# Kernel optimization log

Hardware: AMD Instinct MI355X
Metric: run time of the kernel (lower is better)

## Reference

```python
import jax, jax.numpy as jnp
import numpy as np
import math

B, S, D_MODEL = 4, 2048, 1024
H, D_QK, D_V = 16, 64, 64


def setup_inputs() -> dict:
    key = jax.random.key(0)
    ks = jax.random.split(key, 12)
    s = 0.02
    return {
        "input_q": jax.random.normal(ks[0], (B, S, D_MODEL), jnp.float32),
        "input_k": jax.random.normal(ks[1], (B, S, D_MODEL), jnp.float32),
        "input_v": jax.random.normal(ks[2], (B, S, D_MODEL), jnp.float32),
        # per-head projection weights stacked over heads: [H, out, d_model] (torch Linear layout)
        "WQw": jax.random.normal(ks[3], (H, D_QK, D_MODEL), jnp.float32) * s,
        "WQb": jax.random.normal(ks[4], (H, D_QK), jnp.float32) * s,
        "WKw": jax.random.normal(ks[5], (H, D_QK, D_MODEL), jnp.float32) * s,
        "WKb": jax.random.normal(ks[6], (H, D_QK), jnp.float32) * s,
        "WVw": jax.random.normal(ks[7], (H, D_V, D_MODEL), jnp.float32) * s,
        "WVb": jax.random.normal(ks[8], (H, D_V), jnp.float32) * s,
        # output projection: Linear(H*D_V, D_MODEL)
        "Ww": jax.random.normal(ks[9], (D_MODEL, H * D_V), jnp.float32) * s,
        "Wb": jax.random.normal(ks[10], (D_MODEL,), jnp.float32) * s,
    }


def _mha(input_q, input_k, input_v, WQw, WQb, WKw, WKb, WVw, WVb, Ww, Wb):
    # per-head projections: [B,H,S,d]
    Q = jnp.einsum("bsd,hed->bhse", input_q, WQw) + WQb[None, :, None, :]
    K = jnp.einsum("bsd,hed->bhse", input_k, WKw) + WKb[None, :, None, :]
    V = jnp.einsum("bsd,hvd->bhsv", input_v, WVw) + WVb[None, :, None, :]
    scores = jnp.einsum("bhse,bhte->bhst", Q, K)  # [B,H,S,S]
    # causal mask added BEFORE division by sqrt(d_model), as in original
    causal = jnp.triu(jnp.full((S, S), -jnp.inf, scores.dtype), k=1)
    scores = (scores + causal) / math.sqrt(D_MODEL)  # NOTE: d_model, not d_qk
    attn = jax.nn.softmax(scores, axis=-1)
    ctx = jnp.einsum("bhst,bhtv->bhsv", attn, V)  # [B,H,S,D_V]
    concat = ctx.transpose(0, 2, 1, 3).reshape(B, S, H * D_V)  # head-order concat
    return concat @ Ww.T + Wb


def reference(input_q, input_k, input_v, WQw, WQb, WKw, WKb, WVw, WVb, Ww, Wb):
    return _mha(input_q, input_k, input_v, WQw, WQb, WKw, WKb, WVw, WVb, Ww, Wb)
```

## Files before the change

### kernel.cpp

```cpp
#include <hip/hip_runtime.h>
#include <hip/hip_bf16.h>

typedef __attribute__((ext_vector_type(8))) short bf16x8;
typedef __attribute__((ext_vector_type(4))) float f32x4;
typedef __attribute__((ext_vector_type(16))) float f32x16;
typedef __attribute__((ext_vector_type(4))) unsigned uint4v;

#define MFMA16(a, b, c) __builtin_amdgcn_mfma_f32_16x16x32_bf16(a, b, c, 0, 0, 0)
#define MFMA32(a, b, c) __builtin_amdgcn_mfma_f32_32x32x16_bf16(a, b, c, 0, 0, 0)

__device__ __forceinline__ unsigned short f2bfn(float f) {
#if defined(__gfx950__)
  __bf16 h = (__bf16)f;
  return __builtin_bit_cast(unsigned short, h);
#else
  union { float f; unsigned u; } x; x.f = f;
  unsigned r = x.u + 0x7fffu + ((x.u >> 16) & 1u);
  return (unsigned short)(r >> 16);
#endif
}

__device__ __forceinline__ unsigned cvtpk(float lo, float hi) {
  unsigned w;
  asm("v_cvt_pk_bf16_f32 %0, %1, %2" : "=v"(w) : "v"(lo), "v"(hi));
  return w;
}

__device__ __forceinline__ void cvt_range(const float* __restrict__ s,
                                          unsigned short* __restrict__ d,
                                          int i, int st, int n8) {
  for (; i < n8; i += st) {
    const float4* sp = reinterpret_cast<const float4*>(s) + 2 * (size_t)i;
    float4 a = sp[0], b = sp[1];
    uint4v o;
    o[0] = cvtpk(a.x, a.y); o[1] = cvtpk(a.z, a.w);
    o[2] = cvtpk(b.x, b.y); o[3] = cvtpk(b.z, b.w);
    reinterpret_cast<uint4v*>(d)[i] = o;
  }
}

__global__ void cvt1_kernel(const float* __restrict__ s, unsigned short* __restrict__ d, int n8) {
  cvt_range(s, d, blockIdx.x * blockDim.x + threadIdx.x, gridDim.x * blockDim.x, n8);
}

__global__ void cvt_first_kernel(const float* s0, const float* s1, const float* s2,
                                 const float* s3, unsigned short* d0, unsigned short* d1,
                                 unsigned short* d2, unsigned short* d3, int wn8,
                                 const float* sq, unsigned short* dq, int qn8) {
  const float* s; unsigned short* d; int n8;
  switch (blockIdx.y) {
    case 0: s = s0; d = d0; n8 = wn8; break;
    case 1: s = s1; d = d1; n8 = wn8; break;
    case 2: s = s2; d = d2; n8 = wn8; break;
    case 3: s = s3; d = d3; n8 = wn8; break;
    default: s = sq; d = dq; n8 = qn8; break;
  }
  cvt_range(s, d, blockIdx.x * blockDim.x + threadIdx.x, gridDim.x * blockDim.x, n8);
}

template <int MODE>
__global__ __launch_bounds__(256) void gemm_kernel(
    const unsigned short* __restrict__ Av, const unsigned short* __restrict__ Bv,
    const float* __restrict__ bias, void* __restrict__ outv,
    int M, int N, int K, float oscale, int nshift, int ngemm,
    const float* __restrict__ csrc, unsigned short* __restrict__ cdst, int cn8) {
  constexpr int BM = 128, BN = 128, BK = 64;
  __shared__ __align__(16) unsigned short As[2][BM * BK];
  __shared__ __align__(16) unsigned short Bs[2][BN * BK];
  const int bx = blockIdx.x;
  const int tid = threadIdx.x;
  if (bx >= ngemm) {
    cvt_range(csrc, cdst, (bx - ngemm) * blockDim.x + tid,
              (gridDim.x - ngemm) * blockDim.x, cn8);
    return;
  }
  int sx = bx;
  if (nshift == 3) sx = (bx & 7) * (ngemm >> 3) + (bx >> 3);
  const int lane = tid & 63, wave = tid >> 6;
  const int wr = wave >> 1, wc = wave & 1;
  const int m0 = (sx >> nshift) * BM, n0 = (sx & ((1 << nshift) - 1)) * BN;
  const int rb = lane & 15, g = lane >> 4;
  const int swz = ((lane & 7) ^ ((lane >> 3) & 7)) * 8;
  f32x4 acc[4][4] = {};

  const unsigned short* Ab = Av + (size_t)m0 * K;
  const unsigned short* Bb = Bv + (size_t)n0 * K;

  auto stage = [&](int buf, int k0) {
#pragma unroll
    for (int i = 0; i < 4; ++i) {
      const int c = wave * 256 + i * 64 + lane;
      const int r = c >> 3;
      __builtin_amdgcn_global_load_lds(
          (const __attribute__((address_space(1))) unsigned int*)(Ab + (size_t)r * K + k0 + swz),
          (__attribute__((address_space(3))) unsigned int*)&As[buf][c * 8], 16, 0, 0);
      __builtin_amdgcn_global_load_lds(
          (const __attribute__((address_space(1))) unsigned int*)(Bb + (size_t)r * K + k0 + swz),
          (__attribute__((address_space(3))) unsigned int*)&Bs[buf][c * 8], 16, 0, 0);
    }
  };

  const int nt = K / BK;
  stage(0, 0);
  int cur = 0;
  for (int t = 0; t < nt; ++t) {
    __syncthreads();
    if (t + 1 < nt) stage(cur ^ 1, (t + 1) * BK);
    const unsigned short* A_ = As[cur];
    const unsigned short* B_ = Bs[cur];
#pragma unroll
    for (int kc = 0; kc < 2; ++kc) {
      bf16x8 af[4], bfr[4];
#pragma unroll
      for (int mi = 0; mi < 4; ++mi)
        af[mi] = *reinterpret_cast<const bf16x8*>(
            &A_[(wr * 64 + mi * 16 + rb) * 64 + (((kc * 4 + g) ^ (rb & 7)) * 8)]);
#pragma unroll
      for (int ni = 0; ni < 4; ++ni)
        bfr[ni] = *reinterpret_cast<const bf16x8*>(
            &B_[(wc * 64 + ni * 16 + rb) * 64 + (((kc * 4 + g) ^ (rb & 7)) * 8)]);
#pragma unroll
      for (int mi = 0; mi < 4; ++mi)
#pragma unroll
        for (int ni = 0; ni < 4; ++ni)
          acc[mi][ni] = MFMA16(af[mi], bfr[ni], acc[mi][ni]);
    }
    cur ^= 1;
  }

#pragma unroll
  for (int mi = 0; mi < 4; ++mi) {
#pragma unroll
    for (int ni = 0; ni < 4; ++ni) {
      int col = n0 + wc * 64 + ni * 16 + rb;
      if constexpr (MODE != 2) {
        float bvv = bias[col];
#pragma unroll
        for (int j = 0; j < 4; ++j) {
          int row = m0 + wr * 64 + mi * 16 + g * 4 + j;
          float v = acc[mi][ni][j] + bvv;
          if constexpr (MODE == 0) {
            v *= oscale;
            int b = row >> 11, s = row & 2047;
            int h = col >> 6, e = col & 63;
            ((unsigned short*)outv)[((size_t)(b * 16 + h) * 2048 + s) * 64 + e] = f2bfn(v);
          } else {
            ((float*)outv)[(size_t)row * N + col] = v;
          }
        }
      } else {
        int bb = col >> 11, s = col & 2047;
#pragma unroll
        for (int j = 0; j < 4; ++j) {
          int row = m0 + wr * 64 + mi * 16 + g * 4 + j;
          float v = acc[mi][ni][j] + bias[row];
          int h = row >> 6, e = row & 63;
          ((unsigned short*)outv)[((size_t)(bb * 16 + h) * 64 + e) * 2048 + s] = f2bfn(v);
        }
      }
    }
  }
}

__global__ __launch_bounds__(256) void attn7_kernel(
    const unsigned short* __restrict__ Qp, const unsigned short* __restrict__ Kp,
    const unsigned short* __restrict__ Vtp, unsigned short* __restrict__ ctx) {
  constexpr int S = 2048;
  __shared__ __align__(16) unsigned short Ks[2][64 * 64];
  __shared__ __align__(16) unsigned short Vs[2][64 * 64];
  const int bx = blockIdx.x;
  const int bh = bx & 63;
  const int qti = 15 - (bx >> 6);
  const int tid = threadIdx.x, wave = tid >> 6, lane = tid & 63;
  const int l31 = lane & 31, hb = lane >> 5;
  const int x7 = l31 & 7;
  const int qw = qti * 128 + wave * 32;
  const unsigned short* Qb = Qp + (size_t)bh * S * 64;
  const unsigned short* Kb = Kp + (size_t)bh * S * 64;
  const unsigned short* Vb = Vtp + (size_t)bh * 64 * S;

  bf16x8 qg[4];
#pragma unroll
  for (int kc = 0; kc < 4; ++kc)
    qg[kc] = *reinterpret_cast<const bf16x8*>(
        Qb + (size_t)(qw + l31) * 64 + 16 * kc + 8 * hb);

  bf16x8 ones;
#pragma unroll
  for (int i = 0; i < 8; ++i) ones[i] = (short)0x3F80;

  f32x16 ls = {};
  f32x16 o[2] = {};
  const int sswz = ((lane & 7) ^ (lane >> 3)) * 8;
  const int nt = qti * 2 + 2;

  const int ci0 = wave * 2 * 64 + lane, ci1 = ci0 + 64;
  const int r0 = wave * 16 + (lane >> 3), r1 = r0 + 8;
  const int rs0 = (r0 & 51) | ((r0 & 4) << 1) | ((r0 & 8) >> 1);
  const int rs1 = (r1 & 51) | ((r1 & 4) << 1) | ((r1 & 8) >> 1);
  const unsigned short* ks0 = Kb + (size_t)rs0 * 64 + sswz;
  const unsigned short* ks1 = Kb + (size_t)rs1 * 64 + sswz;
  const unsigned short* vs0 = Vb + (size_t)r0 * S + sswz;
  const unsigned short* vs1 = Vb + (size_t)r1 * S + sswz;

  auto stage = [&](int buf) {
    __builtin_amdgcn_global_load_lds(
        (const __attribute__((address_space(1))) unsigned int*)ks0,
        (__attribute__((address_space(3))) unsigned int*)&Ks[buf][ci0 * 8], 16, 0, 0);
    __builtin_amdgcn_global_load_lds(
        (const __attribute__((address_space(1))) unsigned int*)ks1,
        (__attribute__((address_space(3))) unsigned int*)&Ks[buf][ci1 * 8], 16, 0, 0);
    __builtin_amdgcn_global_load_lds(
        (const __attribute__((address_space(1))) unsigned int*)vs0,
        (__attribute__((address_space(3))) unsigned int*)&Vs[buf][ci0 * 8], 16, 0, 0);
    __builtin_amdgcn_global_load_lds(
        (const __attribute__((address_space(1))) unsigned int*)vs1,
        (__attribute__((address_space(3))) unsigned int*)&Vs[buf][ci1 * 8], 16, 0, 0);
    ks0 += 4096; ks1 += 4096;
    vs0 += 64; vs1 += 64;
  };

  stage(0);

  for (int it = 0; it < nt; ++it) {
    __syncthreads();
    if (it + 1 < nt) stage((it + 1) & 1);
    const int kv0 = 64 * it;
    if (kv0 <= qw + 31) {
      const unsigned short* K_ = Ks[it & 1];
      const unsigned short* V_ = Vs[it & 1];
      f32x16 sacc[2] = {};
      __builtin_amdgcn_s_setprio(1);
#pragma unroll
      for (int kc = 0; kc < 4; ++kc) {
        bf16x8 kf0 = *reinterpret_cast<const bf16x8*>(
            &K_[l31 * 64 + ((2 * kc + hb) ^ x7) * 8]);
        bf16x8 kf1 = *reinterpret_cast<const bf16x8*>(
            &K_[(32 + l31) * 64 + ((2 * kc + hb) ^ x7) * 8]);
        sacc[0] = MFMA32(kf0, qg[kc], sacc[0]);
        sacc[1] = MFMA32(kf1, qg[kc], sacc[1]);
      }
      __builtin_amdgcn_s_setprio(0);
      if (kv0 + 63 > qw) {
        const int qrel = qw + l31 - kv0 - 8 * hb;
#pragma unroll
        for (int mi = 0; mi < 2; ++mi)
#pragma unroll
          for (int r = 0; r < 16; ++r) {
            int koff = (r & 7) + 16 * (r >> 3) + 32 * mi;
            if (koff > qrel) sacc[mi][r] = -1e30f;
          }
      }
      float p0[16], p1[16];
#pragma unroll
      for (int r = 0; r < 16; ++r) p0[r] = __builtin_amdgcn_exp2f(sacc[0][r]);
#pragma unroll
      for (int r = 0; r < 16; ++r) p1[r] = __builtin_amdgcn_exp2f(sacc[1][r]);
      unsigned pw[2][8];
#pragma unroll
      for (int i = 0; i < 8; ++i) pw[0][i] = cvtpk(p0[2 * i], p0[2 * i + 1]);
#pragma unroll
      for (int i = 0; i < 8; ++i) pw[1][i] = cvtpk(p1[2 * i], p1[2 * i + 1]);
      __builtin_amdgcn_s_setprio(1);
#pragma unroll
      for (int c = 0; c < 4; ++c) {
        union { unsigned u[4]; bf16x8 v; } pu;
        pu.u[0] = pw[c >> 1][(c & 1) * 4 + 0];
        pu.u[1] = pw[c >> 1][(c & 1) * 4 + 1];
        pu.u[2] = pw[c >> 1][(c & 1) * 4 + 2];
        pu.u[3] = pw[c >> 1][(c & 1) * 4 + 3];
#pragma unroll
        for (int db = 0; db < 2; ++db) {
          bf16x8 vf = *reinterpret_cast<const bf16x8*>(
              &V_[(32 * db + l31) * 64 + ((2 * c + hb) ^ x7) * 8]);
          o[db] = MFMA32(vf, pu.v, o[db]);
        }
        ls = MFMA32(ones, pu.v, ls);
      }
      __builtin_amdgcn_s_setprio(0);
    }
  }

  const float inv = 1.0f / ls[0];
  const int b = bh >> 4, h = bh & 15;
  const int q = qw + l31;
  unsigned short* cp = ctx + ((size_t)(b * 2048 + q) * 1024) + h * 64;
#pragma unroll
  for (int db = 0; db < 2; ++db)
#pragma unroll
    for (int i = 0; i < 8; ++i) {
      unsigned w = cvtpk(o[db][2 * i] * inv, o[db][2 * i + 1] * inv);
      int d = 32 * db + ((2 * i) & 3) + 8 * (i >> 1) + 4 * hb;
      *reinterpret_cast<unsigned*>(cp + d) = w;
    }
}

extern "C" void kernel_launch(void* const* d_in, const int* in_sizes, int n_in,
                              void* d_out, int out_size, void* d_ws, size_t ws_size,
                              hipStream_t stream) {
  const float* in_q = (const float*)d_in[0];
  const float* in_k = (const float*)d_in[1];
  const float* in_v = (const float*)d_in[2];
  const float* WQw = (const float*)d_in[3];
  const float* WQb = (const float*)d_in[4];
  const float* WKw = (const float*)d_in[5];
  const float* WKb = (const float*)d_in[6];
  const float* WVw = (const float*)d_in[7];
  const float* WVb = (const float*)d_in[8];
  const float* Ww  = (const float*)d_in[9];
  const float* Wb  = (const float*)d_in[10];
  float* out = (float*)d_out;

  constexpr size_t PROJ = (size_t)4 * 16 * 2048 * 64;
  constexpr size_t WSZ = (size_t)1024 * 1024;
  const float qscale = 0.03125f * 1.4426950408889634f;
  unsigned short* wsp = (unsigned short*)d_ws;

  const bool fused = ws_size >= (6 * PROJ + 4 * WSZ) * sizeof(unsigned short);

  if (fused) {
    unsigned short* Qp   = wsp;
    unsigned short* Kp   = wsp + PROJ;
    unsigned short* Vt   = wsp + 2 * PROJ;
    unsigned short* inq  = wsp + 3 * PROJ;
    unsigned short* ctx  = inq;
    unsigned short* ink  = wsp + 4 * PROJ;
    unsigned short* inv  = wsp + 5 * PROJ;
    unsigned short* wq16 = wsp + 6 * PROJ;
    unsigned short* wk16 = wq16 + WSZ;
    unsigned short* wv16 = wk16 + WSZ;
    unsigned short* ww16 = wv16 + WSZ;

    cvt_first_kernel<<<dim3(1024, 5), 256, 0, stream>>>(
        WQw, WKw, WVw, Ww, wq16, wk16, wv16, ww16, (int)(WSZ / 8),
        in_q, inq, (int)(PROJ / 8));
    gemm_kernel<0><<<2560, 256, 0, stream>>>(inq, wq16, WQb, Qp, 8192, 1024, 1024,
                                             qscale, 3, 512, in_k, ink, (int)(PROJ / 8));
    gemm_kernel<0><<<2560, 256, 0, stream>>>(ink, wk16, WKb, Kp, 8192, 1024, 1024,
                                             1.0f, 3, 512, in_v, inv, (int)(PROJ / 8));
    gemm_kernel<2><<<512, 256, 0, stream>>>(wv16, inv, WVb, Vt, 1024, 8192, 1024,
                                            1.0f, 6, 512, nullptr, nullptr, 0);
    attn7_kernel<<<1024, 256, 0, stream>>>(Qp, Kp, Vt, ctx);
    gemm_kernel<1><<<512, 256, 0, stream>>>(ctx, ww16, Wb, out, 8192, 1024, 1024,
                                            1.0f, 3, 512, nullptr, nullptr, 0);
  } else {
    unsigned short* Qp   = wsp;
    unsigned short* Kp   = wsp + PROJ;
    unsigned short* Vt   = wsp + 2 * PROJ;
    unsigned short* in16 = wsp + 3 * PROJ;
    unsigned short* ctx  = in16;
    unsigned short* wq16 = wsp + 4 * PROJ;
    unsigned short* wk16 = wq16 + WSZ;
    unsigned short* wv16 = wk16 + WSZ;
    unsigned short* ww16 = wv16 + WSZ;

    cvt_first_kernel<<<dim3(1024, 5), 256, 0, stream>>>(
        WQw, WKw, WVw, Ww, wq16, wk16, wv16, ww16, (int)(WSZ / 8),
        in_q, in16, (int)(PROJ / 8));
    gemm_kernel<0><<<512, 256, 0, stream>>>(in16, wq16, WQb, Qp, 8192, 1024, 1024,
                                            qscale, 3, 512, nullptr, nullptr, 0);
    cvt1_kernel<<<2048, 256, 0, stream>>>(in_k, in16, (int)(PROJ / 8));
    gemm_kernel<0><<<512, 256, 0, stream>>>(in16, wk16, WKb, Kp, 8192, 1024, 1024,
                                            1.0f, 3, 512, nullptr, nullptr, 0);
    cvt1_kernel<<<2048, 256, 0, stream>>>(in_v, in16, (int)(PROJ / 8));
    gemm_kernel<2><<<512, 256, 0, stream>>>(wv16, in16, WVb, Vt, 1024, 8192, 1024,
                                            1.0f, 6, 512, nullptr, nullptr, 0);
    attn7_kernel<<<1024, 256, 0, stream>>>(Qp, Kp, Vt, ctx);
    gemm_kernel<1><<<512, 256, 0, stream>>>(ctx, ww16, Wb, out, 8192, 1024, 1024,
                                            1.0f, 3, 512, nullptr, nullptr, 0);
  }
}
```

Before: 174.8 us.

## Fuse attention and output projection into one launch with counter-based dependency

Merges the attention kernel and the output projection GEMM into a single launch. Blocks 0-1023 run attention and atomically bump a per-(batch, query-tile) counter after writing ctx, and blocks 1024+ spin-wait on that counter before running the 128x128 output GEMM tile. The goal is to overlap the output projection with the attention tail and drop a kernel boundary. The risks are deadlock if waiting GEMM blocks hold resources before their producers are scheduled, plus spin-wait overhead and a slightly larger workspace requirement that could turn off the fused path.

```diff
diff --git a/kernel.cpp b/kernel.cpp
--- a/kernel.cpp
+++ b/kernel.cpp
@@ -46,7 +46,10 @@
 __global__ void cvt_first_kernel(const float* s0, const float* s1, const float* s2,
                                  const float* s3, unsigned short* d0, unsigned short* d1,
                                  unsigned short* d2, unsigned short* d3, int wn8,
-                                 const float* sq, unsigned short* dq, int qn8) {
+                                 const float* sq, unsigned short* dq, int qn8,
+                                 unsigned* cnt) {
+  if (cnt && blockIdx.x == 0 && blockIdx.y == 0 && threadIdx.x < 64)
+    cnt[threadIdx.x] = 0;
   const float* s; unsigned short* d; int n8;
   switch (blockIdx.y) {
     case 0: s = s0; d = d0; n8 = wn8; break;
@@ -159,6 +162,228 @@
         }
       }
     }
+  }
+}
+
+__global__ __launch_bounds__(256, 4) void attn_gemmo_kernel(
+    const unsigned short* __restrict__ Qp, const unsigned short* __restrict__ Kp,
+    const unsigned short* __restrict__ Vtp, unsigned short* __restrict__ ctx,
+    const unsigned short* __restrict__ Wo, const float* __restrict__ bo,
+    float* __restrict__ out, unsigned* __restrict__ cnt) {
+  constexpr int S = 2048;
+  __shared__ __align__(16) unsigned short smem[16384];
+  const int bx = blockIdx.x;
+  const int tid = threadIdx.x;
+  const int lane = tid & 63, wave = tid >> 6;
+
+  if (bx < 1024) {
+    unsigned short (*Ks)[4096] = reinterpret_cast<unsigned short(*)[4096]>(smem);
+    unsigned short (*Vs)[4096] = reinterpret_cast<unsigned short(*)[4096]>(smem + 8192);
+    const int bh = bx & 63;
+    const int qti = 15 - (bx >> 6);
+    const int l31 = lane & 31, hb = lane >> 5;
+    const int x7 = l31 & 7;
+    const int qw = qti * 128 + wave * 32;
+    const unsigned short* Qb = Qp + (size_t)bh * S * 64;
+    const unsigned short* Kb = Kp + (size_t)bh * S * 64;
+    const unsigned short* Vb = Vtp + (size_t)bh * 64 * S;
+
+    bf16x8 qg[4];
+#pragma unroll
+    for (int kc = 0; kc < 4; ++kc)
+      qg[kc] = *reinterpret_cast<const bf16x8*>(
+          Qb + (size_t)(qw + l31) * 64 + 16 * kc + 8 * hb);
+
+    bf16x8 ones;
+#pragma unroll
+    for (int i = 0; i < 8; ++i) ones[i] = (short)0x3F80;
+
+    f32x16 ls = {};
+    f32x16 o[2] = {};
+    const int sswz = ((lane & 7) ^ (lane >> 3)) * 8;
+    const int nt = qti * 2 + 2;
+
+    const int ci0 = wave * 2 * 64 + lane, ci1 = ci0 + 64;
+    const int r0 = wave * 16 + (lane >> 3), r1 = r0 + 8;
+    const int rs0 = (r0 & 51) | ((r0 & 4) << 1) | ((r0 & 8) >> 1);
+    const int rs1 = (r1 & 51) | ((r1 & 4) << 1) | ((r1 & 8) >> 1);
+    const unsigned short* ks0 = Kb + (size_t)rs0 * 64 + sswz;
+    const unsigned short* ks1 = Kb + (size_t)rs1 * 64 + sswz;
+    const unsigned short* vs0 = Vb + (size_t)r0 * S + sswz;
+    const unsigned short* vs1 = Vb + (size_t)r1 * S + sswz;
+
+    auto stage = [&](int buf) {
+      __builtin_amdgcn_global_load_lds(
+          (const __attribute__((address_space(1))) unsigned int*)ks0,
+          (__attribute__((address_space(3))) unsigned int*)&Ks[buf][ci0 * 8], 16, 0, 0);
+      __builtin_amdgcn_global_load_lds(
+          (const __attribute__((address_space(1))) unsigned int*)ks1,
+          (__attribute__((address_space(3))) unsigned int*)&Ks[buf][ci1 * 8], 16, 0, 0);
+      __builtin_amdgcn_global_load_lds(
+          (const __attribute__((address_space(1))) unsigned int*)vs0,
+          (__attribute__((address_space(3))) unsigned int*)&Vs[buf][ci0 * 8], 16, 0, 0);
+      __builtin_amdgcn_global_load_lds(
+          (const __attribute__((address_space(1))) unsigned int*)vs1,
+          (__attribute__((address_space(3))) unsigned int*)&Vs[buf][ci1 * 8], 16, 0, 0);
+      ks0 += 4096; ks1 += 4096;
+      vs0 += 64; vs1 += 64;
+    };
+
+    stage(0);
+
+    for (int it = 0; it < nt; ++it) {
+      __syncthreads();
+      if (it + 1 < nt) stage((it + 1) & 1);
+      const int kv0 = 64 * it;
+      if (kv0 <= qw + 31) {
+        const unsigned short* K_ = Ks[it & 1];
+        const unsigned short* V_ = Vs[it & 1];
+        f32x16 sacc[2] = {};
+        __builtin_amdgcn_s_setprio(1);
+#pragma unroll
+        for (int kc = 0; kc < 4; ++kc) {
+          bf16x8 kf0 = *reinterpret_cast<const bf16x8*>(
+              &K_[l31 * 64 + ((2 * kc + hb) ^ x7) * 8]);
+          bf16x8 kf1 = *reinterpret_cast<const bf16x8*>(
+              &K_[(32 + l31) * 64 + ((2 * kc + hb) ^ x7) * 8]);
+          sacc[0] = MFMA32(kf0, qg[kc], sacc[0]);
+          sacc[1] = MFMA32(kf1, qg[kc], sacc[1]);
+        }
+        __builtin_amdgcn_s_setprio(0);
+        if (kv0 + 63 > qw) {
+          const int qrel = qw + l31 - kv0 - 8 * hb;
+#pragma unroll
+          for (int mi = 0; mi < 2; ++mi)
+#pragma unroll
+            for (int r = 0; r < 16; ++r) {
+              int koff = (r & 7) + 16 * (r >> 3) + 32 * mi;
+              if (koff > qrel) sacc[mi][r] = -1e30f;
+            }
+        }
+        float p0[16], p1[16];
+#pragma unroll
+        for (int r = 0; r < 16; ++r) p0[r] = __builtin_amdgcn_exp2f(sacc[0][r]);
+#pragma unroll
+        for (int r = 0; r < 16; ++r) p1[r] = __builtin_amdgcn_exp2f(sacc[1][r]);
+        unsigned pw[2][8];
+#pragma unroll
+        for (int i = 0; i < 8; ++i) pw[0][i] = cvtpk(p0[2 * i], p0[2 * i + 1]);
+#pragma unroll
+        for (int i = 0; i < 8; ++i) pw[1][i] = cvtpk(p1[2 * i], p1[2 * i + 1]);
+        __builtin_amdgcn_s_setprio(1);
+#pragma unroll
+        for (int c = 0; c < 4; ++c) {
+          union { unsigned u[4]; bf16x8 v; } pu;
+          pu.u[0] = pw[c >> 1][(c & 1) * 4 + 0];
+          pu.u[1] = pw[c >> 1][(c & 1) * 4 + 1];
+          pu.u[2] = pw[c >> 1][(c & 1) * 4 + 2];
+          pu.u[3] = pw[c >> 1][(c & 1) * 4 + 3];
+#pragma unroll
+          for (int db = 0; db < 2; ++db) {
+            bf16x8 vf = *reinterpret_cast<const bf16x8*>(
+                &V_[(32 * db + l31) * 64 + ((2 * c + hb) ^ x7) * 8]);
+            o[db] = MFMA32(vf, pu.v, o[db]);
+          }
+          ls = MFMA32(ones, pu.v, ls);
+        }
+        __builtin_amdgcn_s_setprio(0);
+      }
+    }
+
+    const float inv = 1.0f / ls[0];
+    const int b = bh >> 4, h = bh & 15;
+    const int q = qw + l31;
+    unsigned short* cp = ctx + ((size_t)(b * 2048 + q) * 1024) + h * 64;
+#pragma unroll
+    for (int db = 0; db < 2; ++db)
+#pragma unroll
+      for (int i = 0; i < 8; ++i) {
+        unsigned w = cvtpk(o[db][2 * i] * inv, o[db][2 * i + 1] * inv);
+        int d = 32 * db + ((2 * i) & 3) + 8 * (i >> 1) + 4 * hb;
+        *reinterpret_cast<unsigned*>(cp + d) = w;
+      }
+
+    __threadfence();
+    __syncthreads();
+    if (tid == 0)
+      __hip_atomic_fetch_add(&cnt[b * 16 + qti], 1u, __ATOMIC_RELEASE,
+                             __HIP_MEMORY_SCOPE_AGENT);
+  } else {
+    unsigned short (*As)[4096] = reinterpret_cast<unsigned short(*)[4096]>(smem);
+    unsigned short (*Bs)[4096] = reinterpret_cast<unsigned short(*)[4096]>(smem + 8192);
+    const int ox = bx - 1024;
+    const int p = ox >> 3;
+    const int qd = p >> 2, bb = p & 3, qti = 15 - qd;
+    const int m0 = bb * 2048 + qti * 128;
+    const int n0 = (ox & 7) * 128;
+    constexpr int K = 1024;
+
+    if (tid == 0) {
+      while (__hip_atomic_load(&cnt[bb * 16 + qti], __ATOMIC_ACQUIRE,
+                               __HIP_MEMORY_SCOPE_AGENT) < 16u)
+        __builtin_amdgcn_s_sleep(16);
+    }
+    __syncthreads();
+    __threadfence();
+
+    const int wr = wave >> 1, wc = wave & 1;
+    const int rb = lane & 15, g = lane >> 4;
+    const int swz = ((lane & 3) ^ ((lane >> 3) & 3)) * 8;
+    const int rk = (rb >> 1) & 3;
+    f32x4 acc[4][4] = {};
+    const unsigned short* Ab = ctx + (size_t)m0 * K;
+    const unsigned short* Bb = Wo + (size_t)n0 * K;
+
+    auto stageO = [&](int buf, int k0) {
+#pragma unroll
+      for (int i = 0; i < 2; ++i) {
+        const int c = wave * 128 + i * 64 + lane;
+        const int r = c >> 2;
+        __builtin_amdgcn_global_load_lds(
+            (const __attribute__((address_space(1))) unsigned int*)(Ab + (size_t)r * K + k0 + swz),
+            (__attribute__((address_space(3))) unsigned int*)&As[buf][c * 8], 16, 0, 0);
+        __builtin_amdgcn_global_load_lds(
+            (const __attribute__((address_space(1))) unsigned int*)(Bb + (size_t)r * K + k0 + swz),
+            (__attribute__((address_space(3))) unsigned int*)&Bs[buf][c * 8], 16, 0, 0);
+      }
+    };
+
+    stageO(0, 0);
+    int cur = 0;
+    for (int t = 0; t < K / 32; ++t) {
+      __syncthreads();
+      if (t + 1 < K / 32) stageO(cur ^ 1, (t + 1) * 32);
+      const unsigned short* A_ = As[cur];
+      const unsigned short* B_ = Bs[cur];
+      bf16x8 af[4], bfr[4];
+#pragma unroll
+      for (int mi = 0; mi < 4; ++mi)
+        af[mi] = *reinterpret_cast<const bf16x8*>(
+            &A_[(wr * 64 + mi * 16 + rb) * 32 + ((g ^ rk) * 8)]);
+#pragma unroll
+      for (int ni = 0; ni < 4; ++ni)
+        bfr[ni] = *reinterpret_cast<const bf16x8*>(
+            &B_[(wc * 64 + ni * 16 + rb) * 32 + ((g ^ rk) * 8)]);
+#pragma unroll
+      for (int mi = 0; mi < 4; ++mi)
+#pragma unroll
+        for (int ni = 0; ni < 4; ++ni)
+          acc[mi][ni] = MFMA16(af[mi], bfr[ni], acc[mi][ni]);
+      cur ^= 1;
+    }
+
+#pragma unroll
+    for (int mi = 0; mi < 4; ++mi)
+#pragma unroll
+      for (int ni = 0; ni < 4; ++ni) {
+        int col = n0 + wc * 64 + ni * 16 + rb;
+        float bvv = bo[col];
+#pragma unroll
+        for (int j = 0; j < 4; ++j) {
+          int row = m0 + wr * 64 + mi * 16 + g * 4 + j;
+          out[(size_t)row * 1024 + col] = acc[mi][ni][j] + bvv;
+        }
+      }
   }
 }
 
@@ -316,7 +541,7 @@
   const float qscale = 0.03125f * 1.4426950408889634f;
   unsigned short* wsp = (unsigned short*)d_ws;
 
-  const bool fused = ws_size >= (6 * PROJ + 4 * WSZ) * sizeof(unsigned short);
+  const bool fused = ws_size >= (6 * PROJ + 4 * WSZ) * sizeof(unsigned short) + 256;
 
   if (fused) {
     unsigned short* Qp   = wsp;
@@ -330,19 +555,18 @@
     unsigned short* wk16 = wq16 + WSZ;
     unsigned short* wv16 = wk16 + WSZ;
     unsigned short* ww16 = wv16 + WSZ;
+    unsigned* cnt = (unsigned*)(ww16 + WSZ);
 
     cvt_first_kernel<<<dim3(1024, 5), 256, 0, stream>>>(
         WQw, WKw, WVw, Ww, wq16, wk16, wv16, ww16, (int)(WSZ / 8),
-        in_q, inq, (int)(PROJ / 8));
+        in_q, inq, (int)(PROJ / 8), cnt);
     gemm_kernel<0><<<2560, 256, 0, stream>>>(inq, wq16, WQb, Qp, 8192, 1024, 1024,
                                              qscale, 3, 512, in_k, ink, (int)(PROJ / 8));
     gemm_kernel<0><<<2560, 256, 0, stream>>>(ink, wk16, WKb, Kp, 8192, 1024, 1024,
                                              1.0f, 3, 512, in_v, inv, (int)(PROJ / 8));
     gemm_kernel<2><<<512, 256, 0, stream>>>(wv16, inv, WVb, Vt, 1024, 8192, 1024,
                                             1.0f, 6, 512, nullptr, nullptr, 0);
-    attn7_kernel<<<1024, 256, 0, stream>>>(Qp, Kp, Vt, ctx);
-    gemm_kernel<1><<<512, 256, 0, stream>>>(ctx, ww16, Wb, out, 8192, 1024, 1024,
-                                            1.0f, 3, 512, nullptr, nullptr, 0);
+    attn_gemmo_kernel<<<1536, 256, 0, stream>>>(Qp, Kp, Vt, ctx, ww16, Wb, out, cnt);
   } else {
     unsigned short* Qp   = wsp;
     unsigned short* Kp   = wsp + PROJ;
@@ -356,7 +580,7 @@
 
     cvt_first_kernel<<<dim3(1024, 5), 256, 0, stream>>>(
         WQw, WKw, WVw, Ww, wq16, wk16, wv16, ww16, (int)(WSZ / 8),
-        in_q, in16, (int)(PROJ / 8));
+        in_q, in16, (int)(PROJ / 8), nullptr);
     gemm_kernel<0><<<512, 256, 0, stream>>>(in16, wq16, WQb, Qp, 8192, 1024, 1024,
                                             qscale, 3, 512, nullptr, nullptr, 0);
     cvt1_kernel<<<2048, 256, 0, stream>>>(in_k, in16, (int)(PROJ / 8));
```

Result: slower. 595.1 us (+240.5%).

## Pair causal query tiles per block to balance attention work

Applied to the files above, without the earlier changes.

Each attention block now handles two query tiles, a late tile (15-pi) and an early tile (pi), so every block does about the same amount of causal work. The grid shrinks from 1024 to 512 blocks, and each staged K/V tile is reused by both query tiles. This removes the tail imbalance of causal attention and halves K/V loads for the early tiles. The cost is twice as many accumulator registers per thread, which may lower occupancy, and fewer blocks in flight.

```diff
diff --git a/kernel.cpp b/kernel.cpp
--- a/kernel.cpp
+++ b/kernel.cpp
@@ -162,7 +162,7 @@
   }
 }
 
-__global__ __launch_bounds__(256) void attn7_kernel(
+__global__ __launch_bounds__(256) void attn8_kernel(
     const unsigned short* __restrict__ Qp, const unsigned short* __restrict__ Kp,
     const unsigned short* __restrict__ Vtp, unsigned short* __restrict__ ctx) {
   constexpr int S = 2048;
@@ -170,29 +170,35 @@
   __shared__ __align__(16) unsigned short Vs[2][64 * 64];
   const int bx = blockIdx.x;
   const int bh = bx & 63;
-  const int qti = 15 - (bx >> 6);
+  const int pi = bx >> 6;
+  const int qtiA = 15 - pi;
+  const int qtiB = pi;
   const int tid = threadIdx.x, wave = tid >> 6, lane = tid & 63;
   const int l31 = lane & 31, hb = lane >> 5;
   const int x7 = l31 & 7;
-  const int qw = qti * 128 + wave * 32;
+  const int qwA = qtiA * 128 + wave * 32;
+  const int qwB = qtiB * 128 + wave * 32;
   const unsigned short* Qb = Qp + (size_t)bh * S * 64;
   const unsigned short* Kb = Kp + (size_t)bh * S * 64;
   const unsigned short* Vb = Vtp + (size_t)bh * 64 * S;
 
-  bf16x8 qg[4];
-#pragma unroll
-  for (int kc = 0; kc < 4; ++kc)
-    qg[kc] = *reinterpret_cast<const bf16x8*>(
-        Qb + (size_t)(qw + l31) * 64 + 16 * kc + 8 * hb);
+  bf16x8 qgA[4], qgB[4];
+#pragma unroll
+  for (int kc = 0; kc < 4; ++kc) {
+    qgA[kc] = *reinterpret_cast<const bf16x8*>(
+        Qb + (size_t)(qwA + l31) * 64 + 16 * kc + 8 * hb);
+    qgB[kc] = *reinterpret_cast<const bf16x8*>(
+        Qb + (size_t)(qwB + l31) * 64 + 16 * kc + 8 * hb);
+  }
 
   bf16x8 ones;
 #pragma unroll
   for (int i = 0; i < 8; ++i) ones[i] = (short)0x3F80;
 
-  f32x16 ls = {};
-  f32x16 o[2] = {};
+  f32x16 lsA = {}, lsB = {};
+  f32x16 oA[2] = {}, oB[2] = {};
   const int sswz = ((lane & 7) ^ (lane >> 3)) * 8;
-  const int nt = qti * 2 + 2;
+  const int nt = qtiA * 2 + 2;
 
   const int ci0 = wave * 2 * 64 + lane, ci1 = ci0 + 64;
   const int r0 = wave * 16 + (lane >> 3), r1 = r0 + 8;
@@ -220,79 +226,95 @@
     vs0 += 64; vs1 += 64;
   };
 
+  auto tile_body = [&](const bf16x8* qg, f32x16* o, f32x16& ls, int qw, int kv0,
+                       const unsigned short* K_, const unsigned short* V_) {
+    f32x16 sacc[2] = {};
+    __builtin_amdgcn_s_setprio(1);
+#pragma unroll
+    for (int kc = 0; kc < 4; ++kc) {
+      bf16x8 kf0 = *reinterpret_cast<const bf16x8*>(
+          &K_[l31 * 64 + ((2 * kc + hb) ^ x7) * 8]);
+      bf16x8 kf1 = *reinterpret_cast<const bf16x8*>(
+          &K_[(32 + l31) * 64 + ((2 * kc + hb) ^ x7) * 8]);
+      sacc[0] = MFMA32(kf0, qg[kc], sacc[0]);
+      sacc[1] = MFMA32(kf1, qg[kc], sacc[1]);
+    }
+    __builtin_amdgcn_s_setprio(0);
+    if (kv0 + 63 > qw) {
+      const int qrel = qw + l31 - kv0 - 8 * hb;
+#pragma unroll
+      for (int mi = 0; mi < 2; ++mi)
+#pragma unroll
+        for (int r = 0; r < 16; ++r) {
+          int koff = (r & 7) + 16 * (r >> 3) + 32 * mi;
+          if (koff > qrel) sacc[mi][r] = -1e30f;
+        }
+    }
+    unsigned pw[2][8];
+#pragma unroll
+    for (int mi = 0; mi < 2; ++mi)
+#pragma unroll
+      for (int i = 0; i < 8; ++i) {
+        float pa = __builtin_amdgcn_exp2f(sacc[mi][2 * i]);
+        float pb = __builtin_amdgcn_exp2f(sacc[mi][2 * i + 1]);
+        pw[mi][i] = cvtpk(pa, pb);
+      }
+    __builtin_amdgcn_s_setprio(1);
+#pragma unroll
+    for (int c = 0; c < 4; ++c) {
+      union { unsigned u[4]; bf16x8 v; } pu;
+      pu.u[0] = pw[c >> 1][(c & 1) * 4 + 0];
+      pu.u[1] = pw[c >> 1][(c & 1) * 4 + 1];
+      pu.u[2] = pw[c >> 1][(c & 1) * 4 + 2];
+      pu.u[3] = pw[c >> 1][(c & 1) * 4 + 3];
+#pragma unroll
+      for (int db = 0; db < 2; ++db) {
+        bf16x8 vf = *reinterpret_cast<const bf16x8*>(
+            &V_[(32 * db + l31) * 64 + ((2 * c + hb) ^ x7) * 8]);
+        o[db] = MFMA32(vf, pu.v, o[db]);
+      }
+      ls = MFMA32(ones, pu.v, ls);
+    }
+    __builtin_amdgcn_s_setprio(0);
+  };
+
   stage(0);
 
   for (int it = 0; it < nt; ++it) {
     __syncthreads();
     if (it + 1 < nt) stage((it + 1) & 1);
     const int kv0 = 64 * it;
-    if (kv0 <= qw + 31) {
-      const unsigned short* K_ = Ks[it & 1];
-      const unsigned short* V_ = Vs[it & 1];
-      f32x16 sacc[2] = {};
-      __builtin_amdgcn_s_setprio(1);
-#pragma unroll
-      for (int kc = 0; kc < 4; ++kc) {
-        bf16x8 kf0 = *reinterpret_cast<const bf16x8*>(
-            &K_[l31 * 64 + ((2 * kc + hb) ^ x7) * 8]);
-        bf16x8 kf1 = *reinterpret_cast<const bf16x8*>(
-            &K_[(32 + l31) * 64 + ((2 * kc + hb) ^ x7) * 8]);
-        sacc[0] = MFMA32(kf0, qg[kc], sacc[0]);
-        sacc[1] = MFMA32(kf1, qg[kc], sacc[1]);
-      }
-      __builtin_amdgcn_s_setprio(0);
-      if (kv0 + 63 > qw) {
-        const int qrel = qw + l31 - kv0 - 8 * hb;
-#pragma unroll
-        for (int mi = 0; mi < 2; ++mi)
-#pragma unroll
-          for (int r = 0; r < 16; ++r) {
-            int koff = (r & 7) + 16 * (r >> 3) + 32 * mi;
-            if (koff > qrel) sacc[mi][r] = -1e30f;
-          }
-      }
-      float p0[16], p1[16];
-#pragma unroll
-      for (int r = 0; r < 16; ++r) p0[r] = __builtin_amdgcn_exp2f(sacc[0][r]);
-#pragma unroll
-      for (int r = 0; r < 16; ++r) p1[r] = __builtin_amdgcn_exp2f(sacc[1][r]);
-      unsigned pw[2][8];
-#pragma unroll
-      for (int i = 0; i < 8; ++i) pw[0][i] = cvtpk(p0[2 * i], p0[2 * i + 1]);
-#pragma unroll
-      for (int i = 0; i < 8; ++i) pw[1][i] = cvtpk(p1[2 * i], p1[2 * i + 1]);
-      __builtin_amdgcn_s_setprio(1);
-#pragma unroll
-      for (int c = 0; c < 4; ++c) {
-        union { unsigned u[4]; bf16x8 v; } pu;
-        pu.u[0] = pw[c >> 1][(c & 1) * 4 + 0];
-        pu.u[1] = pw[c >> 1][(c & 1) * 4 + 1];
-        pu.u[2] = pw[c >> 1][(c & 1) * 4 + 2];
-        pu.u[3] = pw[c >> 1][(c & 1) * 4 + 3];
-#pragma unroll
-        for (int db = 0; db < 2; ++db) {
-          bf16x8 vf = *reinterpret_cast<const bf16x8*>(
-              &V_[(32 * db + l31) * 64 + ((2 * c + hb) ^ x7) * 8]);
-          o[db] = MFMA32(vf, pu.v, o[db]);
-        }
-        ls = MFMA32(ones, pu.v, ls);
-      }
-      __builtin_amdgcn_s_setprio(0);
-    }
-  }
-
-  const float inv = 1.0f / ls[0];
+    const unsigned short* K_ = Ks[it & 1];
+    const unsigned short* V_ = Vs[it & 1];
+    if (kv0 <= qwA + 31) tile_body(qgA, oA, lsA, qwA, kv0, K_, V_);
+    if (kv0 <= qwB + 31) tile_body(qgB, oB, lsB, qwB, kv0, K_, V_);
+  }
+
   const int b = bh >> 4, h = bh & 15;
-  const int q = qw + l31;
-  unsigned short* cp = ctx + ((size_t)(b * 2048 + q) * 1024) + h * 64;
-#pragma unroll
-  for (int db = 0; db < 2; ++db)
-#pragma unroll
-    for (int i = 0; i < 8; ++i) {
-      unsigned w = cvtpk(o[db][2 * i] * inv, o[db][2 * i + 1] * inv);
-      int d = 32 * db + ((2 * i) & 3) + 8 * (i >> 1) + 4 * hb;
-      *reinterpret_cast<unsigned*>(cp + d) = w;
-    }
+  {
+    const float inv = 1.0f / lsA[0];
+    unsigned short* cp = ctx + ((size_t)(b * 2048 + qwA + l31) * 1024) + h * 64;
+#pragma unroll
+    for (int db = 0; db < 2; ++db)
+#pragma unroll
+      for (int i = 0; i < 8; ++i) {
+        unsigned w = cvtpk(oA[db][2 * i] * inv, oA[db][2 * i + 1] * inv);
+        int d = 32 * db + ((2 * i) & 3) + 8 * (i >> 1) + 4 * hb;
+        *reinterpret_cast<unsigned*>(cp + d) = w;
+      }
+  }
+  {
+    const float inv = 1.0f / lsB[0];
+    unsigned short* cp = ctx + ((size_t)(b * 2048 + qwB + l31) * 1024) + h * 64;
+#pragma unroll
+    for (int db = 0; db < 2; ++db)
+#pragma unroll
+      for (int i = 0; i < 8; ++i) {
+        unsigned w = cvtpk(oB[db][2 * i] * inv, oB[db][2 * i + 1] * inv);
+        int d = 32 * db + ((2 * i) & 3) + 8 * (i >> 1) + 4 * hb;
+        *reinterpret_cast<unsigned*>(cp + d) = w;
+      }
+  }
 }
 
 extern "C" void kernel_launch(void* const* d_in, const int* in_sizes, int n_in,
@@ -340,7 +362,7 @@
                                              1.0f, 3, 512, in_v, inv, (int)(PROJ / 8));
     gemm_kernel<2><<<512, 256, 0, stream>>>(wv16, inv, WVb, Vt, 1024, 8192, 1024,
                                             1.0f, 6, 512, nullptr, nullptr, 0);
-    attn7_kernel<<<1024, 256, 0, stream>>>(Qp, Kp, Vt, ctx);
+    attn8_kernel<<<512, 256, 0, stream>>>(Qp, Kp, Vt, ctx);
     gemm_kernel<1><<<512, 256, 0, stream>>>(ctx, ww16, Wb, out, 8192, 1024, 1024,
                                             1.0f, 3, 512, nullptr, nullptr, 0);
   } else {
@@ -365,7 +387,7 @@
     cvt1_kernel<<<2048, 256, 0, stream>>>(in_v, in16, (int)(PROJ / 8));
     gemm_kernel<2><<<512, 256, 0, stream>>>(wv16, in16, WVb, Vt, 1024, 8192, 1024,
                                             1.0f, 6, 512, nullptr, nullptr, 0);
-    attn7_kernel<<<1024, 256, 0, stream>>>(Qp, Kp, Vt, ctx);
+    attn8_kernel<<<512, 256, 0, stream>>>(Qp, Kp, Vt, ctx);
     gemm_kernel<1><<<512, 256, 0, stream>>>(ctx, ww16, Wb, out, 8192, 1024, 1024,
                                             1.0f, 3, 512, nullptr, nullptr, 0);
   }
```

Result: slower. 214.5 us (+22.7%).

## Software-pipeline attention: overlap QK^T of next tile with PV of previous, triple-buffer LDS

Applied to the files above, without the earlier changes.

The attention kernel now uses three LDS buffers for K and V and stages two tiles ahead, waiting on vmcnt explicitly instead of a full __syncthreads. The loop is unrolled by two so the QK^T MFMAs of tile i run alongside the exp/convert and PV MFMAs of tile i-1, hiding softmax ALU latency behind matrix work. The cost is more LDS per block (which can lower occupancy), more live registers for two score accumulators, and extra barriers.

```diff
diff --git a/kernel.cpp b/kernel.cpp
--- a/kernel.cpp
+++ b/kernel.cpp
@@ -162,12 +162,12 @@
   }
 }
 
-__global__ __launch_bounds__(256) void attn7_kernel(
+__global__ __launch_bounds__(256) void attn9_kernel(
     const unsigned short* __restrict__ Qp, const unsigned short* __restrict__ Kp,
     const unsigned short* __restrict__ Vtp, unsigned short* __restrict__ ctx) {
   constexpr int S = 2048;
-  __shared__ __align__(16) unsigned short Ks[2][64 * 64];
-  __shared__ __align__(16) unsigned short Vs[2][64 * 64];
+  __shared__ __align__(16) unsigned short Ks[3][64 * 64];
+  __shared__ __align__(16) unsigned short Vs[3][64 * 64];
   const int bx = blockIdx.x;
   const int bh = bx & 63;
   const int qti = 15 - (bx >> 6);
@@ -220,66 +220,98 @@
     vs0 += 64; vs1 += 64;
   };
 
+  auto qkt = [&](f32x16* sacc, const unsigned short* K_, int kv0) {
+    sacc[0] = f32x16{};
+    sacc[1] = f32x16{};
+    __builtin_amdgcn_s_setprio(1);
+#pragma unroll
+    for (int kc = 0; kc < 4; ++kc) {
+      bf16x8 kf0 = *reinterpret_cast<const bf16x8*>(
+          &K_[l31 * 64 + ((2 * kc + hb) ^ x7) * 8]);
+      bf16x8 kf1 = *reinterpret_cast<const bf16x8*>(
+          &K_[(32 + l31) * 64 + ((2 * kc + hb) ^ x7) * 8]);
+      sacc[0] = MFMA32(kf0, qg[kc], sacc[0]);
+      sacc[1] = MFMA32(kf1, qg[kc], sacc[1]);
+    }
+    __builtin_amdgcn_s_setprio(0);
+    if (kv0 + 63 > qw) {
+      const int qrel = qw + l31 - kv0 - 8 * hb;
+#pragma unroll
+      for (int mi = 0; mi < 2; ++mi)
+#pragma unroll
+        for (int r = 0; r < 16; ++r) {
+          int koff = (r & 7) + 16 * (r >> 3) + 32 * mi;
+          if (koff > qrel) sacc[mi][r] = -1e30f;
+        }
+    }
+  };
+
+  auto finish = [&](const f32x16* sacc, const unsigned short* V_) {
+    unsigned pw[2][8];
+#pragma unroll
+    for (int mi = 0; mi < 2; ++mi)
+#pragma unroll
+      for (int i = 0; i < 8; ++i) {
+        float pa = __builtin_amdgcn_exp2f(sacc[mi][2 * i]);
+        float pb = __builtin_amdgcn_exp2f(sacc[mi][2 * i + 1]);
+        pw[mi][i] = cvtpk(pa, pb);
+      }
+    __builtin_amdgcn_s_setprio(1);
+#pragma unroll
+    for (int c = 0; c < 4; ++c) {
+      union { unsigned u[4]; bf16x8 v; } pu;
+      pu.u[0] = pw[c >> 1][(c & 1) * 4 + 0];
+      pu.u[1] = pw[c >> 1][(c & 1) * 4 + 1];
+      pu.u[2] = pw[c >> 1][(c & 1) * 4 + 2];
+      pu.u[3] = pw[c >> 1][(c & 1) * 4 + 3];
+#pragma unroll
+      for (int db = 0; db < 2; ++db) {
+        bf16x8 vf = *reinterpret_cast<const bf16x8*>(
+            &V_[(32 * db + l31) * 64 + ((2 * c + hb) ^ x7) * 8]);
+        o[db] = MFMA32(vf, pu.v, o[db]);
+      }
+      ls = MFMA32(ones, pu.v, ls);
+    }
+    __builtin_amdgcn_s_setprio(0);
+  };
+
   stage(0);
-
-  for (int it = 0; it < nt; ++it) {
-    __syncthreads();
-    if (it + 1 < nt) stage((it + 1) & 1);
-    const int kv0 = 64 * it;
-    if (kv0 <= qw + 31) {
-      const unsigned short* K_ = Ks[it & 1];
-      const unsigned short* V_ = Vs[it & 1];
-      f32x16 sacc[2] = {};
-      __builtin_amdgcn_s_setprio(1);
-#pragma unroll
-      for (int kc = 0; kc < 4; ++kc) {
-        bf16x8 kf0 = *reinterpret_cast<const bf16x8*>(
-            &K_[l31 * 64 + ((2 * kc + hb) ^ x7) * 8]);
-        bf16x8 kf1 = *reinterpret_cast<const bf16x8*>(
-            &K_[(32 + l31) * 64 + ((2 * kc + hb) ^ x7) * 8]);
-        sacc[0] = MFMA32(kf0, qg[kc], sacc[0]);
-        sacc[1] = MFMA32(kf1, qg[kc], sacc[1]);
+  stage(1);
+
+  f32x16 sA[2], sB[2];
+
+  for (int it = 0; it < nt; it += 2) {
+    if (it < nt - 1) asm volatile("s_waitcnt vmcnt(4)" ::: "memory");
+    else             asm volatile("s_waitcnt vmcnt(0)" ::: "memory");
+    __builtin_amdgcn_s_barrier();
+    __builtin_amdgcn_sched_barrier(0);
+    {
+      const int kv0 = 64 * it;
+      if (kv0 <= qw + 31) qkt(sA, Ks[it % 3], kv0);
+      if (it > 0 && kv0 - 64 <= qw + 31) finish(sB, Vs[(it - 1) % 3]);
+      if (it + 2 < nt) {
+        __builtin_amdgcn_s_barrier();
+        __builtin_amdgcn_sched_barrier(0);
+        stage((it + 2) % 3);
       }
-      __builtin_amdgcn_s_setprio(0);
-      if (kv0 + 63 > qw) {
-        const int qrel = qw + l31 - kv0 - 8 * hb;
-#pragma unroll
-        for (int mi = 0; mi < 2; ++mi)
-#pragma unroll
-          for (int r = 0; r < 16; ++r) {
-            int koff = (r & 7) + 16 * (r >> 3) + 32 * mi;
-            if (koff > qrel) sacc[mi][r] = -1e30f;
-          }
+    }
+    const int it1 = it + 1;
+    if (it1 < nt - 1) asm volatile("s_waitcnt vmcnt(4)" ::: "memory");
+    else              asm volatile("s_waitcnt vmcnt(0)" ::: "memory");
+    __builtin_amdgcn_s_barrier();
+    __builtin_amdgcn_sched_barrier(0);
+    {
+      const int kv0 = 64 * it1;
+      if (kv0 <= qw + 31) qkt(sB, Ks[it1 % 3], kv0);
+      if (kv0 - 64 <= qw + 31) finish(sA, Vs[it % 3]);
+      if (it1 + 2 < nt) {
+        __builtin_amdgcn_s_barrier();
+        __builtin_amdgcn_sched_barrier(0);
+        stage((it1 + 2) % 3);
       }
-      float p0[16], p1[16];
-#pragma unroll
-      for (int r = 0; r < 16; ++r) p0[r] = __builtin_amdgcn_exp2f(sacc[0][r]);
-#pragma unroll
-      for (int r = 0; r < 16; ++r) p1[r] = __builtin_amdgcn_exp2f(sacc[1][r]);
-      unsigned pw[2][8];
-#pragma unroll
-      for (int i = 0; i < 8; ++i) pw[0][i] = cvtpk(p0[2 * i], p0[2 * i + 1]);
-#pragma unroll
-      for (int i = 0; i < 8; ++i) pw[1][i] = cvtpk(p1[2 * i], p1[2 * i + 1]);
-      __builtin_amdgcn_s_setprio(1);
-#pragma unroll
-      for (int c = 0; c < 4; ++c) {
-        union { unsigned u[4]; bf16x8 v; } pu;
-        pu.u[0] = pw[c >> 1][(c & 1) * 4 + 0];
-        pu.u[1] = pw[c >> 1][(c & 1) * 4 + 1];
-        pu.u[2] = pw[c >> 1][(c & 1) * 4 + 2];
-        pu.u[3] = pw[c >> 1][(c & 1) * 4 + 3];
-#pragma unroll
-        for (int db = 0; db < 2; ++db) {
-          bf16x8 vf = *reinterpret_cast<const bf16x8*>(
-              &V_[(32 * db + l31) * 64 + ((2 * c + hb) ^ x7) * 8]);
-          o[db] = MFMA32(vf, pu.v, o[db]);
-        }
-        ls = MFMA32(ones, pu.v, ls);
-      }
-      __builtin_amdgcn_s_setprio(0);
-    }
-  }
+    }
+  }
+  if (64 * (nt - 1) <= qw + 31) finish(sB, Vs[(nt - 1) % 3]);
 
   const float inv = 1.0f / ls[0];
   const int b = bh >> 4, h = bh & 15;
@@ -340,7 +372,7 @@
                                              1.0f, 3, 512, in_v, inv, (int)(PROJ / 8));
     gemm_kernel<2><<<512, 256, 0, stream>>>(wv16, inv, WVb, Vt, 1024, 8192, 1024,
                                             1.0f, 6, 512, nullptr, nullptr, 0);
-    attn7_kernel<<<1024, 256, 0, stream>>>(Qp, Kp, Vt, ctx);
+    attn9_kernel<<<1024, 256, 0, stream>>>(Qp, Kp, Vt, ctx);
     gemm_kernel<1><<<512, 256, 0, stream>>>(ctx, ww16, Wb, out, 8192, 1024, 1024,
                                             1.0f, 3, 512, nullptr, nullptr, 0);
   } else {
@@ -365,7 +397,7 @@
     cvt1_kernel<<<2048, 256, 0, stream>>>(in_v, in16, (int)(PROJ / 8));
     gemm_kernel<2><<<512, 256, 0, stream>>>(wv16, in16, WVb, Vt, 1024, 8192, 1024,
                                             1.0f, 6, 512, nullptr, nullptr, 0);
-    attn7_kernel<<<1024, 256, 0, stream>>>(Qp, Kp, Vt, ctx);
+    attn9_kernel<<<1024, 256, 0, stream>>>(Qp, Kp, Vt, ctx);
     gemm_kernel<1><<<512, 256, 0, stream>>>(ctx, ww16, Wb, out, 8192, 1024, 1024,
                                             1.0f, 3, 512, nullptr, nullptr, 0);
   }
```

Result: faster. 169.7 us, median of 2 (-2.9%).
